# Performance work log

Measured on AMD Instinct MI355X. Metric: run time of the kernel, lower is better.

## Reference

```python
import jax, jax.numpy as jnp
import numpy as np

B, C, N = 16, 128, 2048  # batch, channels (SA_Layer(128)), num points


def setup_inputs() -> dict:
    key = jax.random.key(0)
    ks = jax.random.split(key, 6)
    x = jax.random.normal(ks[0], (B, C, N), jnp.float32)
    wq = jax.random.normal(ks[1], (C // 4, C), jnp.float32) * 0.05  # shared q/k 1x1 conv, no bias
    wv = jax.random.normal(ks[2], (C, C), jnp.float32) * 0.05
    bv = jax.random.normal(ks[3], (C,), jnp.float32) * 0.05
    wt = jax.random.normal(ks[4], (C, C), jnp.float32) * 0.05
    bt = jax.random.normal(ks[5], (C,), jnp.float32) * 0.05
    gamma = jnp.ones((C,), jnp.float32)   # BatchNorm1d weight
    beta = jnp.zeros((C,), jnp.float32)   # BatchNorm1d bias
    bn_mean = jnp.zeros((C,), jnp.float32)  # running mean (eval mode)
    bn_var = jnp.ones((C,), jnp.float32)    # running var (eval mode)
    return dict(x=x, wq=wq, wv=wv, bv=bv, wt=wt, bt=bt,
                gamma=gamma, beta=beta, bn_mean=bn_mean, bn_var=bn_var)


def reference(x, wq, wv, bv, wt, bt, gamma, beta, bn_mean, bn_var):
    EPS = 1e-9
    BN_EPS = 1e-5
    # q_conv and k_conv share weights (tied in __init__)
    x_q = jnp.einsum('dc,bcn->bnd', wq, x)               # [B, N, C/4]
    x_k = jnp.einsum('dc,bcn->bdn', wq, x)               # [B, C/4, N]
    energy = jnp.einsum('bnd,bdm->bnm', x_q, x_k)        # [B, N, N]
    attn = jax.nn.softmax(energy, axis=-1)
    # offset-attention renormalization: divide by column sum
    attn = attn / (EPS + attn.sum(axis=1, keepdims=True))
    x_v = jnp.einsum('dc,bcn->bdn', wv, x) + bv[None, :, None]   # [B, C, N]
    x_r = jnp.einsum('bdn,bnm->bdm', x_v, attn)                  # [B, C, N]
    t = jnp.einsum('dc,bcn->bdn', wt, x - x_r) + bt[None, :, None]
    # BatchNorm1d (eval mode) + ReLU
    t = (t - bn_mean[None, :, None]) * jax.lax.rsqrt(bn_var + BN_EPS)[None, :, None]
    t = t * gamma[None, :, None] + beta[None, :, None]
    return x + jax.nn.relu(t)
```

## Files before the change

kernel.cpp:

```cpp
#include <hip/hip_runtime.h>
#include <hip/hip_bf16.h>
#include <math.h>

#define BB 16
#define CC 128
#define NN 2048
#define CQ 32

typedef __attribute__((ext_vector_type(8))) short bf16x8;
typedef __attribute__((ext_vector_type(4))) float f32x4;
typedef __attribute__((ext_vector_type(16))) float f32x16;
typedef unsigned char uchar;

__device__ __forceinline__ ushort f2b(float f) {
    __hip_bfloat16 h = __float2bfloat16(f);
    return *reinterpret_cast<ushort*>(&h);
}
__device__ __forceinline__ float b2f(ushort u) {
    union { unsigned u; float f; } v; v.u = ((unsigned)u) << 16;
    return v.f;
}
__device__ __forceinline__ uint f2q4(float a, float b, float c, float d) {
    int r = __builtin_amdgcn_cvt_pk_fp8_f32(a, b, 0, false);
    r = __builtin_amdgcn_cvt_pk_fp8_f32(c, d, r, true);
    return (uint)r;
}
__device__ __forceinline__ bf16x8 as_b8(uint4 u) {
    union { uint4 u; bf16x8 b; } v; v.u = u; return v.b;
}
__device__ __forceinline__ bf16x8 as_b8_2(uint2 a, uint2 b) {
    return as_b8(make_uint4(a.x, a.y, b.x, b.y));
}
__device__ __forceinline__ float fexp2(float x) {
    return __builtin_amdgcn_exp2f(x);
}
union U2L { uint2 u; long l; };

#define OFF_VB  524288
#define OFF_RSI 4718592

#define QSCALE 1.2011224087864498f

__global__ __launch_bounds__(256) void k_proj(const float* __restrict__ x,
        const float* __restrict__ wq, const float* __restrict__ wv,
        const float* __restrict__ bv, ushort* __restrict__ Qt, uchar* __restrict__ Vb) {
    __shared__ ushort Wl[160][136];
    __shared__ ushort Xs[64][136];
    int bid = (blockIdx.x & 7) * 64 + (blockIdx.x >> 3);
    int b  = bid >> 5;
    int n0 = (bid & 31) << 6;
    int tid = threadIdx.x;
    #pragma unroll
    for (int k = 0; k < 20; ++k) {
        int idx = k * 256 + tid;
        int r = idx >> 5, c4 = (idx & 31) << 2;
        const float* srcw = (r < 32) ? (wq + r * 128 + c4) : (wv + (r - 32) * 128 + c4);
        float4 w4 = *(const float4*)srcw;
        float s = (r < 32) ? QSCALE : 1.0f;
        *(ushort4*)&Wl[r][c4] = make_ushort4(f2b(w4.x * s), f2b(w4.y * s),
                                             f2b(w4.z * s), f2b(w4.w * s));
    }
    const float* xb = x + (size_t)b * CC * NN;
    for (int idx = tid; idx < 2048; idx += 256) {
        int c = idx >> 4, n4 = (idx & 15) << 2;
        float4 xv = *(const float4*)&xb[c * NN + n0 + n4];
        Xs[n4][c]     = f2b(xv.x);
        Xs[n4 + 1][c] = f2b(xv.y);
        Xs[n4 + 2][c] = f2b(xv.z);
        Xs[n4 + 3][c] = f2b(xv.w);
    }
    __syncthreads();
    int w = tid >> 6, l = tid & 63, lr = l & 15, lg = l >> 4;
    f32x4 zero = {0.f, 0.f, 0.f, 0.f};
    int nn = n0 + w * 16 + lr;
    for (int dt = 0; dt < 10; ++dt) {
        f32x4 acc = zero;
        #pragma unroll
        for (int k = 0; k < 4; ++k) {
            bf16x8 a  = *(const bf16x8*)&Wl[dt * 16 + lr][k * 32 + lg * 8];
            bf16x8 bx = *(const bf16x8*)&Xs[w * 16 + lr][k * 32 + lg * 8];
            acc = __builtin_amdgcn_mfma_f32_16x16x32_bf16(a, bx, acc, 0, 0, 0);
        }
        if (dt < 2) {
            ushort4 p = make_ushort4(f2b(acc[0]), f2b(acc[1]), f2b(acc[2]), f2b(acc[3]));
            *(ushort4*)&Qt[(size_t)(b * NN + nn) * CQ + dt * 16 + lg * 4] = p;
        } else {
            union { uint u; uchar c[4]; } q;
            int vd = (dt - 2) * 16 + lg * 4;
            q.u = f2q4(acc[0] + bv[vd], acc[1] + bv[vd + 1],
                       acc[2] + bv[vd + 2], acc[3] + bv[vd + 3]);
            #pragma unroll
            for (int i = 0; i < 4; ++i)
                Vb[(size_t)(b * CC + vd + i) * NN + nn] = q.c[i];
        }
    }
}

__global__ __launch_bounds__(512) void k_rowstats(const ushort* __restrict__ Qt,
        float* __restrict__ RSI) {
    __shared__ ushort Qm[128][36];
    __shared__ float Sred[2][64];
    int bid = (blockIdx.x & 7) * 64 + (blockIdx.x >> 3);
    int b  = bid >> 5;
    int n0 = (bid & 31) << 6;
    int tid = threadIdx.x;
    int w = tid >> 6, l = tid & 63, lr = l & 15, lg = l >> 4;
    int wn = w & 3, wm = w >> 2;
    const ushort* Qtb = Qt + (size_t)b * NN * CQ;
    bf16x8 aq = *(const bf16x8*)&Qtb[(size_t)(n0 + wn * 16 + lr) * CQ + lg * 8];
    int sr = tid >> 2, sc = (tid & 3) * 8;
    uint4 q0 = *(const uint4*)&Qtb[(size_t)sr * CQ + sc];
    float S[4] = {0.f, 0.f, 0.f, 0.f};
    f32x4 zero = {0.f, 0.f, 0.f, 0.f};
    for (int t = 0; t < 16; ++t) {
        __syncthreads();
        *(uint4*)&Qm[sr][sc] = q0;
        __syncthreads();
        if (t < 15)
            q0 = *(const uint4*)&Qtb[(size_t)((t + 1) * 128 + sr) * CQ + sc];
        #pragma unroll
        for (int mi = 0; mi < 4; ++mi) {
            bf16x8 bq = *(const bf16x8*)&Qm[(wm * 4 + mi) * 16 + lr][lg * 8];
            f32x4 e = __builtin_amdgcn_mfma_f32_16x16x32_bf16(aq, bq, zero, 0, 0, 0);
            S[0] += fexp2(e[0]); S[1] += fexp2(e[1]);
            S[2] += fexp2(e[2]); S[3] += fexp2(e[3]);
        }
    }
    #pragma unroll
    for (int d = 1; d < 16; d <<= 1) {
        #pragma unroll
        for (int i = 0; i < 4; ++i) S[i] += __shfl_xor(S[i], d);
    }
    if (lr == 0) {
        #pragma unroll
        for (int i = 0; i < 4; ++i) Sred[wm][wn * 16 + lg * 4 + i] = S[i];
    }
    __syncthreads();
    if (tid < 64)
        RSI[b * NN + n0 + tid] = 256.f / (Sred[0][tid] + Sred[1][tid]);
}

__global__ __launch_bounds__(768, 3) void k_attn_pv(const ushort* __restrict__ Qt,
        const uchar* __restrict__ Vb, const float* __restrict__ RSI,
        const float* __restrict__ x, const float* __restrict__ wt,
        const float* __restrict__ bt, const float* __restrict__ gamma,
        const float* __restrict__ beta, const float* __restrict__ bn_mean,
        const float* __restrict__ bn_var, float* __restrict__ out) {
    __shared__ uchar SMp[2][2][128][72];
    __shared__ ushort wtl[16896];
    __shared__ float csred[4][128];
    __shared__ float csum[128];
    __shared__ float fAl[128], fBl[128];
    int bid = (blockIdx.x & 7) * 32 + (blockIdx.x >> 3);
    int b  = bid >> 4;
    int m0 = (bid & 15) << 7;
    int tid = threadIdx.x;
    int w = tid >> 6, l = tid & 63, lr = l & 15, lg = l >> 4;
    const ushort* Qtb = Qt + (size_t)b * NN * CQ;
    const uchar*  Vbb = Vb + (size_t)b * CC * NN;
    const float*  RSb = RSI + (size_t)b * NN;
    const float*  xb  = x   + (size_t)b * CC * NN;
    float*        outb = out + (size_t)b * CC * NN;
    f32x4 zero = {0.f, 0.f, 0.f, 0.f};
    bool producer = (w < 4);

    for (int idx = tid; idx < 4096; idx += 768) {
        int r = idx >> 5, c4 = (idx & 31) << 2;
        float4 w4 = *(const float4*)&wt[r * 128 + c4];
        *(ushort4*)&wtl[r * 132 + c4] =
            make_ushort4(f2b(w4.x), f2b(w4.y), f2b(w4.z), f2b(w4.w));
    }
    if (tid < 128) {
        float A = gamma[tid] * rsqrtf(bn_var[tid] + 1e-5f);
        fAl[tid] = A;
        fBl[tid] = (bt[tid] - bn_mean[tid]) * A + beta[tid];
    }

    int wn = w;
    bf16x8 bm[8];
    float cs[8] = {0.f, 0.f, 0.f, 0.f, 0.f, 0.f, 0.f, 0.f};
    int sv = 0, shv = 0;
    const uchar* vsrc = nullptr;
    bf16x8 aq_nx; float4 rsi_nx;
    int cw = w - 4;
    int dq = cw >> 1, mh2 = cw & 1;
    int ar = l & 31, kh = l >> 5;
    f32x16 pacc0, pacc1;

    if (producer) {
        #pragma unroll
        for (int mi = 0; mi < 8; ++mi)
            bm[mi] = *(const bf16x8*)&Qtb[(size_t)(m0 + mi * 16 + lr) * CQ + lg * 8];
        sv = tid >> 1; shv = (tid & 1) * 32;
        vsrc = Vbb + (size_t)sv * NN + shv;
        {
            uint4 v0 = *(const uint4*)(vsrc);
            uint4 v1 = *(const uint4*)(vsrc + 16);
            uchar* dst = &SMp[0][0][sv][shv];
            *(uint2*)(dst)      = make_uint2(v0.x, v0.y);
            *(uint2*)(dst + 8)  = make_uint2(v0.z, v0.w);
            *(uint2*)(dst + 16) = make_uint2(v1.x, v1.y);
            *(uint2*)(dst + 24) = make_uint2(v1.z, v1.w);
        }
        {
            bf16x8 aq0 = *(const bf16x8*)&Qtb[(size_t)(wn * 16 + lr) * CQ + lg * 8];
            float4 r4 = *(const float4*)&RSb[wn * 16 + lg * 4];
            int nb = wn * 16 + lg * 4;
            #pragma unroll
            for (int mi = 0; mi < 8; ++mi) {
                f32x4 e = __builtin_amdgcn_mfma_f32_16x16x32_bf16(aq0, bm[mi], zero, 0, 0, 0);
                float w0 = fexp2(e[0]) * r4.x;
                float w1 = fexp2(e[1]) * r4.y;
                float w2 = fexp2(e[2]) * r4.z;
                float w3 = fexp2(e[3]) * r4.w;
                cs[mi] += w0 + w1 + w2 + w3;
                *(uint*)&SMp[1][0][mi * 16 + lr][nb] = f2q4(w0, w1, w2, w3);
            }
        }
        aq_nx  = *(const bf16x8*)&Qtb[(size_t)(64 + wn * 16 + lr) * CQ + lg * 8];
        rsi_nx = *(const float4*)&RSb[64 + wn * 16 + lg * 4];
    } else {
        #pragma unroll
        for (int r = 0; r < 16; ++r) { pacc0[r] = 0.f; pacc1[r] = 0.f; }
    }
    __syncthreads();
    for (int t = 0; t < 32; ++t) {
        int cur = t & 1;
        if (producer) {
            if (t < 31) {
                int ntn = (t + 1) * 64;
                uint4 v0 = *(const uint4*)(vsrc + ntn);
                uint4 v1 = *(const uint4*)(vsrc + ntn + 16);
                bf16x8 aq = aq_nx;
                float4 r4 = rsi_nx;
                if (t < 30) {
                    int nt2 = (t + 2) * 64;
                    aq_nx  = *(const bf16x8*)&Qtb[(size_t)(nt2 + wn * 16 + lr) * CQ + lg * 8];
                    rsi_nx = *(const float4*)&RSb[nt2 + wn * 16 + lg * 4];
                }
                int nb = wn * 16 + lg * 4;
                #pragma unroll
                for (int mi = 0; mi < 8; ++mi) {
                    f32x4 e = __builtin_amdgcn_mfma_f32_16x16x32_bf16(aq, bm[mi], zero, 0, 0, 0);
                    float w0 = fexp2(e[0]) * r4.x;
                    float w1 = fexp2(e[1]) * r4.y;
                    float w2 = fexp2(e[2]) * r4.z;
                    float w3 = fexp2(e[3]) * r4.w;
                    cs[mi] += w0 + w1 + w2 + w3;
                    *(uint*)&SMp[1][cur ^ 1][mi * 16 + lr][nb] = f2q4(w0, w1, w2, w3);
                }
                uchar* dst = &SMp[0][cur ^ 1][sv][shv];
                *(uint2*)(dst)      = make_uint2(v0.x, v0.y);
                *(uint2*)(dst + 8)  = make_uint2(v0.z, v0.w);
                *(uint2*)(dst + 16) = make_uint2(v1.x, v1.y);
                *(uint2*)(dst + 24) = make_uint2(v1.z, v1.w);
            }
        } else {
            __builtin_amdgcn_s_setprio(1);
            #pragma unroll
            for (int kk = 0; kk < 4; ++kk) {
                int cb = kk * 16 + kh * 8;
                U2L va, wb0, wb1;
                va.u  = *(const uint2*)&SMp[0][cur][dq * 32 + ar][cb];
                wb0.u = *(const uint2*)&SMp[1][cur][mh2 * 64 + ar][cb];
                wb1.u = *(const uint2*)&SMp[1][cur][mh2 * 64 + 32 + ar][cb];
                pacc0 = __builtin_amdgcn_mfma_f32_32x32x16_fp8_fp8(va.l, wb0.l, pacc0, 0, 0, 0);
                pacc1 = __builtin_amdgcn_mfma_f32_32x32x16_fp8_fp8(va.l, wb1.l, pacc1, 0, 0, 0);
            }
            __builtin_amdgcn_s_setprio(0);
        }
        __syncthreads();
    }
    if (producer) {
        #pragma unroll
        for (int mi = 0; mi < 8; ++mi) {
            cs[mi] += __shfl_xor(cs[mi], 16);
            cs[mi] += __shfl_xor(cs[mi], 32);
        }
        if (lg == 0) {
            #pragma unroll
            for (int mi = 0; mi < 8; ++mi)
                csred[wn][mi * 16 + lr] = cs[mi];
        }
    }
    __syncthreads();
    if (tid < 128) {
        float tot = csred[0][tid] + csred[1][tid] + csred[2][tid] + csred[3][tid];
        csum[tid] = 1.f / (2.56e-7f + tot);
    }
    __syncthreads();
    ushort* UsP = (ushort*)&SMp[0][0][0][0];
    if (!producer) {
        float inv0 = csum[mh2 * 64 + ar];
        float inv1 = csum[mh2 * 64 + 32 + ar];
        int mA = m0 + mh2 * 64 + ar;
        int mL = mh2 * 64 + ar;
        #pragma unroll
        for (int g = 0; g < 4; ++g) {
            int db = dq * 32 + 8 * g + 4 * kh;
            ushort4 u0, u1;
            #pragma unroll
            for (int j = 0; j < 4; ++j) {
                int r = 4 * g + j;
                float x0 = xb[(size_t)(db + j) * NN + mA];
                float x1 = xb[(size_t)(db + j) * NN + mA + 32];
                ((ushort*)&u0)[j] = f2b(x0 - pacc0[r] * inv0);
                ((ushort*)&u1)[j] = f2b(x1 - pacc1[r] * inv1);
            }
            *(ushort4*)&UsP[mL * 132 + db]        = u0;
            *(ushort4*)&UsP[(mL + 32) * 132 + db] = u1;
        }
    }
    __syncthreads();
    for (int tile = w; tile < 16; tile += 12) {
        int rt = tile >> 2, mt = tile & 3;
        f32x16 acc;
        #pragma unroll
        for (int r = 0; r < 16; ++r) acc[r] = 0.f;
        #pragma unroll
        for (int kk = 0; kk < 8; ++kk) {
            const ushort* ap = &wtl[(rt * 32 + ar) * 132 + kk * 16 + kh * 8];
            uint2 a0 = *(const uint2*)ap; uint2 a1 = *(const uint2*)(ap + 4);
            const ushort* bp = &UsP[(mt * 32 + ar) * 132 + kk * 16 + kh * 8];
            uint2 b0 = *(const uint2*)bp; uint2 b1 = *(const uint2*)(bp + 4);
            acc = __builtin_amdgcn_mfma_f32_32x32x16_bf16(
                as_b8_2(a0, a1), as_b8_2(b0, b1), acc, 0, 0, 0);
        }
        int m = m0 + mt * 32 + ar;
        #pragma unroll
        for (int g = 0; g < 4; ++g) {
            #pragma unroll
            for (int j = 0; j < 4; ++j) {
                int r = rt * 32 + j + 8 * g + 4 * kh;
                float t = acc[4 * g + j] * fAl[r] + fBl[r];
                t = fmaxf(t, 0.f);
                outb[(size_t)r * NN + m] = xb[(size_t)r * NN + m] + t;
            }
        }
    }
}

extern "C" void kernel_launch(void* const* d_in, const int* in_sizes, int n_in,
                              void* d_out, int out_size, void* d_ws, size_t ws_size,
                              hipStream_t stream) {
    const float* x       = (const float*)d_in[0];
    const float* wq      = (const float*)d_in[1];
    const float* wv      = (const float*)d_in[2];
    const float* bv      = (const float*)d_in[3];
    const float* wt      = (const float*)d_in[4];
    const float* bt      = (const float*)d_in[5];
    const float* gamma   = (const float*)d_in[6];
    const float* beta    = (const float*)d_in[7];
    const float* bn_mean = (const float*)d_in[8];
    const float* bn_var  = (const float*)d_in[9];
    float* out = (float*)d_out;
    float* ws  = (float*)d_ws;

    ushort* Qt   = (ushort*)ws;
    uchar*  Vbp  = (uchar*)(ws + OFF_VB);
    float*  RSI  = ws + OFF_RSI;

    k_proj<<<BB * 32, 256, 0, stream>>>(x, wq, wv, bv, Qt, Vbp);
    k_rowstats<<<BB * 32, 512, 0, stream>>>(Qt, RSI);
    k_attn_pv<<<BB * 16, 768, 0, stream>>>(Qt, Vbp, RSI, x, wt, bt, gamma, beta,
                                           bn_mean, bn_var, out);
}
```

Baseline: 60.33 us.

## Halve attention-PV column tile to 64, doubling block count with 512 threads

Shrinks each attention×V block's output column tile from 128 to 64 columns. The launch now has 512 blocks of 512 threads (4 producer and 4 consumer waves) instead of 256 blocks of 768 threads. Each consumer wave now owns one 32-row channel slice across all 64 columns. This should fill more of the MI355X's CUs, since 256 blocks under-occupy the device. In exchange, each V tile is streamed from global memory twice as many times overall, and the per-block weight-to-LDS conversion of wt is repeated in twice as many blocks.

```diff
diff --git a/kernel.cpp b/kernel.cpp
--- a/kernel.cpp
+++ b/kernel.cpp
@@ -140,20 +140,21 @@
         RSI[b * NN + n0 + tid] = 256.f / (Sred[0][tid] + Sred[1][tid]);
 }
 
-__global__ __launch_bounds__(768, 3) void k_attn_pv(const ushort* __restrict__ Qt,
+__global__ __launch_bounds__(512, 4) void k_attn_pv(const ushort* __restrict__ Qt,
         const uchar* __restrict__ Vb, const float* __restrict__ RSI,
         const float* __restrict__ x, const float* __restrict__ wt,
         const float* __restrict__ bt, const float* __restrict__ gamma,
         const float* __restrict__ beta, const float* __restrict__ bn_mean,
         const float* __restrict__ bn_var, float* __restrict__ out) {
-    __shared__ uchar SMp[2][2][128][72];
+    __shared__ uchar Vsm[2][128][72];
+    __shared__ uchar Wsm[2][64][72];
     __shared__ ushort wtl[16896];
-    __shared__ float csred[4][128];
-    __shared__ float csum[128];
+    __shared__ float csred[4][64];
+    __shared__ float csum[64];
     __shared__ float fAl[128], fBl[128];
-    int bid = (blockIdx.x & 7) * 32 + (blockIdx.x >> 3);
-    int b  = bid >> 4;
-    int m0 = (bid & 15) << 7;
+    int bid = (blockIdx.x & 7) * 64 + (blockIdx.x >> 3);
+    int b  = bid >> 5;
+    int m0 = (bid & 31) << 6;
     int tid = threadIdx.x;
     int w = tid >> 6, l = tid & 63, lr = l & 15, lg = l >> 4;
     const ushort* Qtb = Qt + (size_t)b * NN * CQ;
@@ -164,7 +165,7 @@
     f32x4 zero = {0.f, 0.f, 0.f, 0.f};
     bool producer = (w < 4);
 
-    for (int idx = tid; idx < 4096; idx += 768) {
+    for (int idx = tid; idx < 4096; idx += 512) {
         int r = idx >> 5, c4 = (idx & 31) << 2;
         float4 w4 = *(const float4*)&wt[r * 128 + c4];
         *(ushort4*)&wtl[r * 132 + c4] =
@@ -177,26 +178,25 @@
     }
 
     int wn = w;
-    bf16x8 bm[8];
-    float cs[8] = {0.f, 0.f, 0.f, 0.f, 0.f, 0.f, 0.f, 0.f};
+    bf16x8 bm[4];
+    float cs[4] = {0.f, 0.f, 0.f, 0.f};
     int sv = 0, shv = 0;
     const uchar* vsrc = nullptr;
     bf16x8 aq_nx; float4 rsi_nx;
     int cw = w - 4;
-    int dq = cw >> 1, mh2 = cw & 1;
     int ar = l & 31, kh = l >> 5;
     f32x16 pacc0, pacc1;
 
     if (producer) {
         #pragma unroll
-        for (int mi = 0; mi < 8; ++mi)
+        for (int mi = 0; mi < 4; ++mi)
             bm[mi] = *(const bf16x8*)&Qtb[(size_t)(m0 + mi * 16 + lr) * CQ + lg * 8];
         sv = tid >> 1; shv = (tid & 1) * 32;
         vsrc = Vbb + (size_t)sv * NN + shv;
         {
             uint4 v0 = *(const uint4*)(vsrc);
             uint4 v1 = *(const uint4*)(vsrc + 16);
-            uchar* dst = &SMp[0][0][sv][shv];
+            uchar* dst = &Vsm[0][sv][shv];
             *(uint2*)(dst)      = make_uint2(v0.x, v0.y);
             *(uint2*)(dst + 8)  = make_uint2(v0.z, v0.w);
             *(uint2*)(dst + 16) = make_uint2(v1.x, v1.y);
@@ -207,14 +207,14 @@
             float4 r4 = *(const float4*)&RSb[wn * 16 + lg * 4];
             int nb = wn * 16 + lg * 4;
             #pragma unroll
-            for (int mi = 0; mi < 8; ++mi) {
+            for (int mi = 0; mi < 4; ++mi) {
                 f32x4 e = __builtin_amdgcn_mfma_f32_16x16x32_bf16(aq0, bm[mi], zero, 0, 0, 0);
                 float w0 = fexp2(e[0]) * r4.x;
                 float w1 = fexp2(e[1]) * r4.y;
                 float w2 = fexp2(e[2]) * r4.z;
                 float w3 = fexp2(e[3]) * r4.w;
                 cs[mi] += w0 + w1 + w2 + w3;
-                *(uint*)&SMp[1][0][mi * 16 + lr][nb] = f2q4(w0, w1, w2, w3);
+                *(uint*)&Wsm[0][mi * 16 + lr][nb] = f2q4(w0, w1, w2, w3);
             }
         }
         aq_nx  = *(const bf16x8*)&Qtb[(size_t)(64 + wn * 16 + lr) * CQ + lg * 8];
@@ -240,16 +240,16 @@
                 }
                 int nb = wn * 16 + lg * 4;
                 #pragma unroll
-                for (int mi = 0; mi < 8; ++mi) {
+                for (int mi = 0; mi < 4; ++mi) {
                     f32x4 e = __builtin_amdgcn_mfma_f32_16x16x32_bf16(aq, bm[mi], zero, 0, 0, 0);
                     float w0 = fexp2(e[0]) * r4.x;
                     float w1 = fexp2(e[1]) * r4.y;
                     float w2 = fexp2(e[2]) * r4.z;
                     float w3 = fexp2(e[3]) * r4.w;
                     cs[mi] += w0 + w1 + w2 + w3;
-                    *(uint*)&SMp[1][cur ^ 1][mi * 16 + lr][nb] = f2q4(w0, w1, w2, w3);
+                    *(uint*)&Wsm[cur ^ 1][mi * 16 + lr][nb] = f2q4(w0, w1, w2, w3);
                 }
-                uchar* dst = &SMp[0][cur ^ 1][sv][shv];
+                uchar* dst = &Vsm[cur ^ 1][sv][shv];
                 *(uint2*)(dst)      = make_uint2(v0.x, v0.y);
                 *(uint2*)(dst + 8)  = make_uint2(v0.z, v0.w);
                 *(uint2*)(dst + 16) = make_uint2(v1.x, v1.y);
@@ -261,9 +261,9 @@
             for (int kk = 0; kk < 4; ++kk) {
                 int cb = kk * 16 + kh * 8;
                 U2L va, wb0, wb1;
-                va.u  = *(const uint2*)&SMp[0][cur][dq * 32 + ar][cb];
-                wb0.u = *(const uint2*)&SMp[1][cur][mh2 * 64 + ar][cb];
-                wb1.u = *(const uint2*)&SMp[1][cur][mh2 * 64 + 32 + ar][cb];
+                va.u  = *(const uint2*)&Vsm[cur][cw * 32 + ar][cb];
+                wb0.u = *(const uint2*)&Wsm[cur][ar][cb];
+                wb1.u = *(const uint2*)&Wsm[cur][32 + ar][cb];
                 pacc0 = __builtin_amdgcn_mfma_f32_32x32x16_fp8_fp8(va.l, wb0.l, pacc0, 0, 0, 0);
                 pacc1 = __builtin_amdgcn_mfma_f32_32x32x16_fp8_fp8(va.l, wb1.l, pacc1, 0, 0, 0);
             }
@@ -273,31 +273,30 @@
     }
     if (producer) {
         #pragma unroll
-        for (int mi = 0; mi < 8; ++mi) {
+        for (int mi = 0; mi < 4; ++mi) {
             cs[mi] += __shfl_xor(cs[mi], 16);
             cs[mi] += __shfl_xor(cs[mi], 32);
         }
         if (lg == 0) {
             #pragma unroll
-            for (int mi = 0; mi < 8; ++mi)
+            for (int mi = 0; mi < 4; ++mi)
                 csred[wn][mi * 16 + lr] = cs[mi];
         }
     }
     __syncthreads();
-    if (tid < 128) {
+    if (tid < 64) {
         float tot = csred[0][tid] + csred[1][tid] + csred[2][tid] + csred[3][tid];
         csum[tid] = 1.f / (2.56e-7f + tot);
     }
     __syncthreads();
-    ushort* UsP = (ushort*)&SMp[0][0][0][0];
+    ushort* UsP = (ushort*)&Vsm[0][0][0];
     if (!producer) {
-        float inv0 = csum[mh2 * 64 + ar];
-        float inv1 = csum[mh2 * 64 + 32 + ar];
-        int mA = m0 + mh2 * 64 + ar;
-        int mL = mh2 * 64 + ar;
+        float inv0 = csum[ar];
+        float inv1 = csum[32 + ar];
+        int mA = m0 + ar;
         #pragma unroll
         for (int g = 0; g < 4; ++g) {
-            int db = dq * 32 + 8 * g + 4 * kh;
+            int db = cw * 32 + 8 * g + 4 * kh;
             ushort4 u0, u1;
             #pragma unroll
             for (int j = 0; j < 4; ++j) {
@@ -307,13 +306,13 @@
                 ((ushort*)&u0)[j] = f2b(x0 - pacc0[r] * inv0);
                 ((ushort*)&u1)[j] = f2b(x1 - pacc1[r] * inv1);
             }
-            *(ushort4*)&UsP[mL * 132 + db]        = u0;
-            *(ushort4*)&UsP[(mL + 32) * 132 + db] = u1;
-        }
-    }
-    __syncthreads();
-    for (int tile = w; tile < 16; tile += 12) {
-        int rt = tile >> 2, mt = tile & 3;
+            *(ushort4*)&UsP[ar * 132 + db]        = u0;
+            *(ushort4*)&UsP[(32 + ar) * 132 + db] = u1;
+        }
+    }
+    __syncthreads();
+    {
+        int rt = w >> 1, mt = w & 1;
         f32x16 acc;
         #pragma unroll
         for (int r = 0; r < 16; ++r) acc[r] = 0.f;
@@ -362,6 +361,6 @@
 
     k_proj<<<BB * 32, 256, 0, stream>>>(x, wq, wv, bv, Qt, Vbp);
     k_rowstats<<<BB * 32, 512, 0, stream>>>(Qt, RSI);
-    k_attn_pv<<<BB * 16, 768, 0, stream>>>(Qt, Vbp, RSI, x, wt, bt, gamma, beta,
+    k_attn_pv<<<BB * 32, 512, 0, stream>>>(Qt, Vbp, RSI, x, wt, bt, gamma, beta,
                                            bn_mean, bn_var, out);
 }
```

Measured after the change: 57.14 us. 1.06x faster.
